# Kernel optimization log

Hardware: AMD Instinct MI355X
Metric: run time of the kernel (lower is better)

## Reference

```python
import jax, jax.numpy as jnp
import numpy as np

DEPTH = 10                      # levels per complete binary tree (node_order in [0, DEPTH-1])
N_TREES = 512
NODES_PER_TREE = 2 ** DEPTH - 1  # 1023
N_FEAT = 64
N_HIDDEN = 64


def _build_forest():
    """Forest of N_TREES complete binary trees, heap-indexed within each tree.

    node_order: 0 at leaves, DEPTH-1 at root (pytorch-tree-lstm convention).
    adjacency_list: (parent, child) pairs, parents grouped consecutively.
    edge_order: node_order of the parent of each edge.
    """
    npt = NODES_PER_TREE
    idx = np.arange(npt)
    level = np.floor(np.log2(idx + 1)).astype(np.int64)   # 0 at root
    order = (DEPTH - 1) - level                            # 0 at leaves
    internal = idx[2 * idx + 2 < npt]
    parents = np.repeat(internal, 2)
    children = np.empty_like(parents)
    children[0::2] = 2 * internal + 1
    children[1::2] = 2 * internal + 2
    base_adj = np.stack([parents, children], axis=1)       # [e, 2]
    eorder = order[parents]
    off = (np.arange(N_TREES) * npt).astype(np.int64)
    node_order = np.tile(order, N_TREES)
    adj = (base_adj[None, :, :] + off[:, None, None]).reshape(-1, 2)
    edge_order = np.tile(eorder, N_TREES)
    return node_order, adj, edge_order


def setup_inputs() -> dict:
    key = jax.random.key(0)
    ks = jax.random.split(key, 10)
    node_order, adj, edge_order = _build_forest()
    N = N_TREES * NODES_PER_TREE
    H, F = N_HIDDEN, N_FEAT
    s_in = 1.0 / np.sqrt(F)
    s_h = 1.0 / np.sqrt(H)
    return {
        "features": jax.random.normal(ks[0], (N, F), jnp.float32),
        "node_order": jnp.asarray(node_order),
        "adjacency_list": jnp.asarray(adj),
        "edge_order": jnp.asarray(edge_order),
        "w_iou": jax.random.normal(ks[1], (3 * H, F), jnp.float32) * s_in,
        "b_iou": jnp.zeros((3 * H,), jnp.float32),
        "u_iou": jax.random.normal(ks[2], (3 * H, H), jnp.float32) * s_h,
        "w_f": jax.random.normal(ks[3], (H, F), jnp.float32) * s_in,
        "b_f": jnp.zeros((H,), jnp.float32),
        "u_f": jax.random.normal(ks[4], (H, H), jnp.float32) * s_h,
        "lin0_w": jax.random.normal(ks[5], (H, H), jnp.float32) * s_h,
        "lin0_b": jnp.zeros((H,), jnp.float32),
        "lin1_w": jax.random.normal(ks[6], (H, H), jnp.float32) * s_h,
        "lin1_b": jnp.zeros((H,), jnp.float32),
        "out_w": jax.random.normal(ks[7], (1, H), jnp.float32) * s_h,
        "out_b": jnp.zeros((1,), jnp.float32),
    }


def _tree_lstm(features, node_order, parent, child, edge_order,
               w_iou, b_iou, u_iou, w_f, b_f, u_f):
    N = features.shape[0]
    H = u_f.shape[0]
    # input contributions are level-independent: compute once for all nodes
    iou_x = features @ w_iou.T + b_iou   # [N, 3H]
    f_x = features @ w_f.T + b_f         # [N, H]
    h = jnp.zeros((N, H), features.dtype)
    c = jnp.zeros((N, H), features.dtype)
    for n in range(DEPTH):               # dependency-chained level sweep
        nmask = (node_order == n)[:, None]
        emask = (edge_order == n)[:, None].astype(features.dtype)
        child_h = h[child]               # [E, H] gather
        child_c = c[child]
        # sum of children h per parent, restricted to this level's edges
        h_sum = jax.ops.segment_sum(child_h * emask, parent, num_segments=N)
        iou = iou_x + h_sum @ u_iou.T
        i, o, u = jnp.split(iou, 3, axis=1)
        i = jax.nn.sigmoid(i)
        o = jax.nn.sigmoid(o)
        u = jnp.tanh(u)
        # per-edge forget gates; contributions masked to this level's edges
        f = jax.nn.sigmoid(f_x[parent] + child_h @ u_f.T)
        c_sum = jax.ops.segment_sum(f * child_c * emask, parent, num_segments=N)
        c = jnp.where(nmask, i * u + c_sum, c)
        h = jnp.where(nmask, o * jnp.tanh(c), h)
    return h, c


def reference(features, node_order, adjacency_list, edge_order,
              w_iou, b_iou, u_iou, w_f, b_f, u_f,
              lin0_w, lin0_b, lin1_w, lin1_b, out_w, out_b):
    parent = adjacency_list[:, 0]
    child = adjacency_list[:, 1]
    h, _ = _tree_lstm(features, node_order, parent, child, edge_order,
                      w_iou, b_iou, u_iou, w_f, b_f, u_f)
    # unbatch + mean pool per tree (all trees have equal size -> reshape)
    x = h.reshape(N_TREES, NODES_PER_TREE, -1).mean(axis=1)
    x = jax.nn.relu(x)                   # dropout is identity in eval mode
    x = jax.nn.relu(x @ lin0_w.T + lin0_b)
    x = jax.nn.relu(x @ lin1_w.T + lin1_b)
    return (x @ out_w.T + out_b).ravel()  # [N_TREES]
```

## Files before the change

### kernel.cpp

```cpp
#include <hip/hip_runtime.h>
#include <math.h>

#define NTREES 512
#define DEPTH  10
#define NPT    1023
#define NTOT   (NTREES * NPT)
#define H      64
#define PART_SLOTS 32256

typedef __attribute__((ext_vector_type(8))) short bf16x8;
typedef __attribute__((ext_vector_type(4))) float f32x4;

__device__ __forceinline__ float sigm(float x)  { return __builtin_amdgcn_rcpf(1.0f + __expf(-x)); }
__device__ __forceinline__ float ftanh(float x) { return fmaf(-2.0f, __builtin_amdgcn_rcpf(__expf(2.0f * x) + 1.0f), 1.0f); }

__device__ __forceinline__ unsigned short bf_hi(float f) {
    unsigned u = __float_as_uint(f);
    return (unsigned short)((u + 0x7fffu + ((u >> 16) & 1u)) >> 16);
}
__device__ __forceinline__ float bf_f(unsigned short h) {
    return __uint_as_float(((unsigned)h) << 16);
}
__device__ __forceinline__ void split8(const float v[8], bf16x8& hi, bf16x8& lo) {
    #pragma unroll
    for (int e = 0; e < 8; ++e) {
        unsigned short hh = bf_hi(v[e]);
        hi[e] = (short)hh;
        lo[e] = (short)bf_hi(v[e] - bf_f(hh));
    }
}

#define MFMA(a, b, c) __builtin_amdgcn_mfma_f32_16x16x32_bf16((a), (b), (c), 0, 0, 0)

__global__ void prep_b(const float* __restrict__ w_iou, const float* __restrict__ u_iou,
                       const float* __restrict__ w_f,  const float* __restrict__ u_f,
                       unsigned short* __restrict__ B)
{
    int idx  = blockIdx.x * 256 + threadIdx.x;
    int unit = idx >> 3;
    int e    = idx & 7;
    int l    = unit & 63;
    float v;
    int hl;
    if (unit < 6144) {
        int sp = (unit >= 3072) ? 1 : 0;
        int r  = unit - sp * 3072;
        int q  = r >> 6;
        hl     = q & 1;
        int ts = q >> 1;
        int s_ = ts & 1;
        int t  = ts >> 1;
        int s  = sp * 2 + s_;
        int col = t * 16 + (l & 15);
        int k   = 32 * s + 8 * (l >> 4) + e;
        v = (k < 64) ? w_iou[col * H + k] : u_iou[col * H + (k - 64)];
    } else {
        int r  = unit - 6144;
        int q  = r >> 6;
        hl     = q & 1;
        int xu = (q >> 1) & 1;
        int ts = q >> 2;
        int s  = ts & 1;
        int t  = ts >> 1;
        int col = t * 16 + (l & 15);
        int k   = 32 * s + 8 * (l >> 4) + e;
        v = xu ? u_f[col * H + k] : w_f[col * H + k];
    }
    unsigned short hv = bf_hi(v);
    B[idx] = hl ? bf_hi(v - bf_f(hv)) : hv;
}

__device__ __forceinline__ void store_partial(float psum[4], int l, int wid,
                                              float* __restrict__ partw)
{
    #pragma unroll
    for (int t = 0; t < 4; ++t) {
        float v = psum[t];
        v += __shfl_xor(v, 16);
        v += __shfl_xor(v, 32);
        if (l < 16) partw[(size_t)wid * H + 16 * t + l] = v;
    }
}

__global__ __launch_bounds__(256, 3)
void leaf_mfma(const float* __restrict__ feat, const unsigned short* __restrict__ Braw,
               const float* __restrict__ b_iou,
               float* __restrict__ h, float* __restrict__ c,
               float* __restrict__ partw, int do_part)
{
    __shared__ bf16x8 Bs[3072];
    int tid = threadIdx.x;
    int l   = tid & 63;
    int w   = tid >> 6;
    int base = blockIdx.x * 64 + w * 16;
    int g    = base + (l & 15);
    int nrow = (g >> 9) * NPT + 511 + (g & 511);
    int ko   = 8 * (l >> 4);

    const float* fb = feat + (size_t)nrow * H + ko;
    float4 fr0 = *(const float4*)(fb);
    float4 fr1 = *(const float4*)(fb + 4);
    float4 fr2 = *(const float4*)(fb + 32);
    float4 fr3 = *(const float4*)(fb + 36);

    const bf16x8* Bg = (const bf16x8*)Braw;
    for (int u = tid; u < 3072; u += 256) Bs[u] = Bg[u];
    __syncthreads();

    bf16x8 fh[2], fl[2];
    { float v[8] = {fr0.x,fr0.y,fr0.z,fr0.w,fr1.x,fr1.y,fr1.z,fr1.w}; split8(v, fh[0], fl[0]); }
    { float v[8] = {fr2.x,fr2.y,fr2.z,fr2.w,fr3.x,fr3.y,fr3.z,fr3.w}; split8(v, fh[1], fl[1]); }

    f32x4 acc[12];
    #pragma unroll
    for (int t = 0; t < 12; ++t) acc[t] = (f32x4){0.f,0.f,0.f,0.f};
    #pragma unroll
    for (int t = 0; t < 12; ++t) {
        #pragma unroll
        for (int s = 0; s < 2; ++s) {
            bf16x8 bh = Bs[((t * 2 + s) * 2 + 0) * 64 + l];
            bf16x8 bl = Bs[((t * 2 + s) * 2 + 1) * 64 + l];
            acc[t] = MFMA(fh[s], bh, acc[t]);
            acc[t] = MFMA(fh[s], bl, acc[t]);
            acc[t] = MFMA(fl[s], bh, acc[t]);
        }
    }
    int colb = l & 15;
    float psum[4] = {0.f, 0.f, 0.f, 0.f};
    #pragma unroll
    for (int r = 0; r < 4; ++r) {
        int gr = base + (l >> 4) * 4 + r;
        int nr = (gr >> 9) * NPT + 511 + (gr & 511);
        #pragma unroll
        for (int t = 0; t < 4; ++t) {
            int j = 16 * t + colb;
            float ai = acc[t][r]     + b_iou[j];
            float ao = acc[4 + t][r] + b_iou[64 + j];
            float au = acc[8 + t][r] + b_iou[128 + j];
            float cv = sigm(ai) * ftanh(au);
            float hval = sigm(ao) * ftanh(cv);
            c[(size_t)nr * H + j] = cv;
            h[(size_t)nr * H + j] = hval;
            psum[t] += hval;
        }
    }
    if (do_part) store_partial(psum, l, blockIdx.x * 4 + w, partw);
}

__global__ __launch_bounds__(256, 3)
void internal_mfma(const float* __restrict__ feat, const unsigned short* __restrict__ Braw,
                   const float* __restrict__ b_iou, const float* __restrict__ b_f,
                   float* __restrict__ h, float* __restrict__ c, int lvl,
                   float* __restrict__ partw, int woff)
{
    __shared__ bf16x8 Bs[3072];
    int tid = threadIdx.x;
    int l   = tid & 63;
    int w   = tid >> 6;
    int m   = 1 << lvl;
    int base  = blockIdx.x * 64 + w * 16;
    int g     = base + (l & 15);
    int tree  = g >> lvl, i = g & (m - 1);
    int local = (m - 1) + i;
    int nrow  = tree * NPT + local;
    int crow0 = tree * NPT + 2 * local + 1;
    int ko    = 8 * (l >> 4);
    int colb  = l & 15;

    const float* fb  = feat + (size_t)nrow * H + ko;
    float4 fr0 = *(const float4*)(fb);
    float4 fr1 = *(const float4*)(fb + 4);
    float4 fr2 = *(const float4*)(fb + 32);
    float4 fr3 = *(const float4*)(fb + 36);
    const float* h0b = h + (size_t)crow0 * H + ko;
    const float* h1b = h0b + H;
    float4 a00 = *(const float4*)(h0b);
    float4 a01 = *(const float4*)(h0b + 4);
    float4 a02 = *(const float4*)(h0b + 32);
    float4 a03 = *(const float4*)(h0b + 36);
    float4 a10 = *(const float4*)(h1b);
    float4 a11 = *(const float4*)(h1b + 4);
    float4 a12 = *(const float4*)(h1b + 32);
    float4 a13 = *(const float4*)(h1b + 36);

    const bf16x8* Bg = (const bf16x8*)Braw;
    for (int u = tid; u < 2048; u += 256) Bs[u] = Bg[6144 + u];
    __syncthreads();

    bf16x8 fh[2], fl[2], sh[2], sl[2], zh[2], zl[2];
    { float v[8] = {fr0.x,fr0.y,fr0.z,fr0.w,fr1.x,fr1.y,fr1.z,fr1.w}; split8(v, fh[0], fl[0]); }
    { float v[8] = {fr2.x,fr2.y,fr2.z,fr2.w,fr3.x,fr3.y,fr3.z,fr3.w}; split8(v, fh[1], fl[1]); }
    {
        float v0[8] = {a00.x,a00.y,a00.z,a00.w,a01.x,a01.y,a01.z,a01.w};
        float v1[8] = {a10.x,a10.y,a10.z,a10.w,a11.x,a11.y,a11.z,a11.w};
        float vs[8];
        #pragma unroll
        for (int e = 0; e < 8; ++e) vs[e] = v0[e] + v1[e];
        split8(v0, zh[0], zl[0]); split8(vs, sh[0], sl[0]);
    }
    {
        float v0[8] = {a02.x,a02.y,a02.z,a02.w,a03.x,a03.y,a03.z,a03.w};
        float v1[8] = {a12.x,a12.y,a12.z,a12.w,a13.x,a13.y,a13.z,a13.w};
        float vs[8];
        #pragma unroll
        for (int e = 0; e < 8; ++e) vs[e] = v0[e] + v1[e];
        split8(v0, zh[1], zl[1]); split8(vs, sh[1], sl[1]);
    }

    float f0[4][4], f1[4][4];
    #pragma unroll
    for (int t = 0; t < 4; ++t) {
        f32x4 ax  = (f32x4){0.f,0.f,0.f,0.f};
        f32x4 as_ = (f32x4){0.f,0.f,0.f,0.f};
        f32x4 az  = (f32x4){0.f,0.f,0.f,0.f};
        #pragma unroll
        for (int s = 0; s < 2; ++s) {
            int qb = (t * 2 + s) * 4;
            bf16x8 bxh = Bs[(qb + 0) * 64 + l];
            bf16x8 bxl = Bs[(qb + 1) * 64 + l];
            bf16x8 buh = Bs[(qb + 2) * 64 + l];
            bf16x8 bul = Bs[(qb + 3) * 64 + l];
            ax  = MFMA(fh[s], bxh, ax);  ax  = MFMA(fh[s], bxl, ax);  ax  = MFMA(fl[s], bxh, ax);
            as_ = MFMA(sh[s], buh, as_); as_ = MFMA(sh[s], bul, as_); as_ = MFMA(sl[s], buh, as_);
            az  = MFMA(zh[s], buh, az);  az  = MFMA(zh[s], bul, az);  az  = MFMA(zl[s], buh, az);
        }
        #pragma unroll
        for (int r = 0; r < 4; ++r) {
            float afx = ax[r] + b_f[16 * t + colb];
            f0[t][r] = sigm(afx + az[r]);
            f1[t][r] = sigm(afx + (as_[r] - az[r]));
        }
    }
    __syncthreads();

    for (int u = tid; u < 3072; u += 256) Bs[u] = Bg[u];
    __syncthreads();
    f32x4 acc[12];
    #pragma unroll
    for (int t = 0; t < 12; ++t) acc[t] = (f32x4){0.f,0.f,0.f,0.f};
    #pragma unroll
    for (int t = 0; t < 12; ++t) {
        #pragma unroll
        for (int s = 0; s < 2; ++s) {
            bf16x8 bh = Bs[((t * 2 + s) * 2 + 0) * 64 + l];
            bf16x8 bl = Bs[((t * 2 + s) * 2 + 1) * 64 + l];
            acc[t] = MFMA(fh[s], bh, acc[t]);
            acc[t] = MFMA(fh[s], bl, acc[t]);
            acc[t] = MFMA(fl[s], bh, acc[t]);
        }
    }
    __syncthreads();

    for (int u = tid; u < 3072; u += 256) Bs[u] = Bg[3072 + u];
    __syncthreads();
    #pragma unroll
    for (int t = 0; t < 12; ++t) {
        #pragma unroll
        for (int s = 0; s < 2; ++s) {
            bf16x8 bh = Bs[((t * 2 + s) * 2 + 0) * 64 + l];
            bf16x8 bl = Bs[((t * 2 + s) * 2 + 1) * 64 + l];
            acc[t] = MFMA(sh[s], bh, acc[t]);
            acc[t] = MFMA(sh[s], bl, acc[t]);
            acc[t] = MFMA(sl[s], bh, acc[t]);
        }
    }

    float psum[4] = {0.f, 0.f, 0.f, 0.f};
    #pragma unroll
    for (int r = 0; r < 4; ++r) {
        int gr = base + (l >> 4) * 4 + r;
        int treer = gr >> lvl, ir = gr & (m - 1);
        int lr = (m - 1) + ir;
        int nr = treer * NPT + lr;
        size_t ch0 = (size_t)(treer * NPT + 2 * lr + 1) * H;
        size_t ch1 = ch0 + H;
        #pragma unroll
        for (int t = 0; t < 4; ++t) {
            int j = 16 * t + colb;
            float ai = acc[t][r]     + b_iou[j];
            float ao = acc[4 + t][r] + b_iou[64 + j];
            float au = acc[8 + t][r] + b_iou[128 + j];
            float cv = sigm(ai) * ftanh(au) + f0[t][r] * c[ch0 + j] + f1[t][r] * c[ch1 + j];
            float hval = sigm(ao) * ftanh(cv);
            c[(size_t)nr * H + j] = cv;
            h[(size_t)nr * H + j] = hval;
            psum[t] += hval;
        }
    }
    if (woff >= 0) store_partial(psum, l, woff + blockIdx.x * 4 + w, partw);
}

__global__ __launch_bounds__(64)
void final_mlp(const float* __restrict__ h, const float* __restrict__ partw,
               const float* __restrict__ l0w, const float* __restrict__ l0b,
               const float* __restrict__ l1w, const float* __restrict__ l1b,
               const float* __restrict__ ow,  const float* __restrict__ ob,
               float* __restrict__ out)
{
    int tree = blockIdx.x;
    int f = threadIdx.x;
    float s = 0.0f;
    #pragma unroll 4
    for (int k = 0; k < 32; ++k) s += partw[(size_t)(tree * 32 + k) * H + f];
    #pragma unroll 4
    for (int k = 0; k < 16; ++k) s += partw[(size_t)(16384 + tree * 16 + k) * H + f];
    #pragma unroll
    for (int k = 0; k < 8; ++k)  s += partw[(size_t)(24576 + tree * 8 + k) * H + f];
    #pragma unroll
    for (int k = 0; k < 4; ++k)  s += partw[(size_t)(28672 + tree * 4 + k) * H + f];
    #pragma unroll
    for (int k = 0; k < 2; ++k)  s += partw[(size_t)(30720 + tree * 2 + k) * H + f];
    s += partw[(size_t)(31744 + tree) * H + f];
    const float* hb = h + (size_t)tree * NPT * H;
    #pragma unroll
    for (int i = 0; i < 15; ++i) s += hb[i * H + f];
    float x = fmaxf(s * (1.0f / 1023.0f), 0.0f);

    __shared__ float xb[H];
    __shared__ float yb[H];
    xb[f] = x;
    __syncthreads();
    float acc = l0b[f];
    #pragma unroll
    for (int k = 0; k < H; ++k) acc = fmaf(l0w[f * H + k], xb[k], acc);
    acc = fmaxf(acc, 0.0f);
    yb[f] = acc;
    __syncthreads();
    float acc2 = l1b[f];
    #pragma unroll
    for (int k = 0; k < H; ++k) acc2 = fmaf(l1w[f * H + k], yb[k], acc2);
    acc2 = fmaxf(acc2, 0.0f);
    float t = ow[f] * acc2;
    #pragma unroll
    for (int off = 32; off > 0; off >>= 1) t += __shfl_down(t, off);
    if (f == 0) out[tree] = t + ob[0];
}

__global__ __launch_bounds__(256)
void pool_kernel(const float* __restrict__ h, float* __restrict__ x)
{
    __shared__ float red[4][H];
    int tree = blockIdx.x;
    int f = threadIdx.x & 63;
    int seg = threadIdx.x >> 6;
    const float* basep = h + (size_t)tree * NPT * H;
    int i0 = seg * 256, i1 = i0 + 256; if (i1 > NPT) i1 = NPT;
    float s = 0.f;
    for (int i = i0; i < i1; ++i) s += basep[i * H + f];
    red[seg][f] = s;
    __syncthreads();
    if (seg == 0) {
        float tot = red[0][f] + red[1][f] + red[2][f] + red[3][f];
        x[tree * H + f] = fmaxf(tot * (1.0f / 1023.0f), 0.0f);
    }
}

__global__ __launch_bounds__(64)
void mlp_kernel(const float* __restrict__ x,
                const float* __restrict__ l0w, const float* __restrict__ l0b,
                const float* __restrict__ l1w, const float* __restrict__ l1b,
                const float* __restrict__ ow,  const float* __restrict__ ob,
                float* __restrict__ out)
{
    int tree = blockIdx.x;
    int j = threadIdx.x;
    __shared__ float xb[H];
    __shared__ float yb[H];
    xb[j] = x[tree * H + j];
    __syncthreads();
    float acc = l0b[j];
    #pragma unroll
    for (int k = 0; k < H; ++k) acc = fmaf(l0w[j * H + k], xb[k], acc);
    acc = fmaxf(acc, 0.0f);
    yb[j] = acc;
    __syncthreads();
    float acc2 = l1b[j];
    #pragma unroll
    for (int k = 0; k < H; ++k) acc2 = fmaf(l1w[j * H + k], yb[k], acc2);
    acc2 = fmaxf(acc2, 0.0f);
    float t = ow[j] * acc2;
    #pragma unroll
    for (int off = 32; off > 0; off >>= 1) t += __shfl_down(t, off);
    if (j == 0) out[tree] = t + ob[0];
}

extern "C" void kernel_launch(void* const* d_in, const int* in_sizes, int n_in,
                              void* d_out, int out_size, void* d_ws, size_t ws_size,
                              hipStream_t stream)
{
    const float* feat  = (const float*)d_in[0];
    const float* w_iou = (const float*)d_in[4];
    const float* b_iou = (const float*)d_in[5];
    const float* u_iou = (const float*)d_in[6];
    const float* w_f   = (const float*)d_in[7];
    const float* b_f   = (const float*)d_in[8];
    const float* u_f   = (const float*)d_in[9];
    const float* l0w   = (const float*)d_in[10];
    const float* l0b   = (const float*)d_in[11];
    const float* l1w   = (const float*)d_in[12];
    const float* l1b   = (const float*)d_in[13];
    const float* ow    = (const float*)d_in[14];
    const float* ob    = (const float*)d_in[15];
    float* out = (float*)d_out;

    float* h = (float*)d_ws;
    float* c = h + (size_t)NTOT * H;
    float* x = c + (size_t)NTOT * H;
    unsigned short* Bf = (unsigned short*)(x + NTREES * H);
    float* partw = (float*)(Bf + 65536);
    size_t needed = (size_t)((char*)(partw + (size_t)PART_SLOTS * H) - (char*)d_ws);
    int use_part = (ws_size >= needed) ? 1 : 0;

    prep_b<<<256, 256, 0, stream>>>(w_iou, u_iou, w_f, u_f, Bf);
    leaf_mfma<<<4096, 256, 0, stream>>>(feat, Bf, b_iou, h, c, partw, use_part);
    for (int lvl = DEPTH - 2; lvl >= 0; --lvl) {
        int woff = (use_part && lvl >= 4) ? (32768 - (64 << lvl)) : -1;
        internal_mfma<<<8 << lvl, 256, 0, stream>>>(
            feat, Bf, b_iou, b_f, h, c, lvl, partw, woff);
    }
    if (use_part) {
        final_mlp<<<NTREES, 64, 0, stream>>>(h, partw, l0w, l0b, l1w, l1b, ow, ob, out);
    } else {
        pool_kernel<<<NTREES, 256, 0, stream>>>(h, x);
        mlp_kernel<<<NTREES, 64, 0, stream>>>(x, l0w, l0b, l1w, l1b, ow, ob, out);
    }
}
```

Before: 318.4 us.

## Fuse the four smallest tree levels into one persistent kernel

Replaces the four separate internal_mfma launches for tree levels 3..0 with one small_levels kernel of 32 blocks. Each block owns a fixed set of 16 trees, stages the full bf16 weight matrix in 128 KB of LDS, and steps through the levels with __syncthreads between them. This cuts three kernel launches and their gaps, plus repeated weight loads, on levels that have very little parallel work. The cost is low occupancy: only 32 blocks run, and at each lower level more warps sit idle.

```diff
diff --git a/kernel.cpp b/kernel.cpp
--- a/kernel.cpp
+++ b/kernel.cpp
@@ -290,6 +290,144 @@
     if (woff >= 0) store_partial(psum, l, woff + blockIdx.x * 4 + w, partw);
 }
 
+__global__ __launch_bounds__(512)
+void small_levels(const float* __restrict__ feat, const unsigned short* __restrict__ Braw,
+                  const float* __restrict__ b_iou, const float* __restrict__ b_f,
+                  float* __restrict__ h, float* __restrict__ c)
+{
+    extern __shared__ bf16x8 Bs[];
+    const bf16x8* Bg = (const bf16x8*)Braw;
+    int tid = threadIdx.x;
+    for (int u = tid; u < 8192; u += 512) Bs[u] = Bg[u];
+    __syncthreads();
+
+    int l    = tid & 63;
+    int w    = tid >> 6;
+    int colb = l & 15;
+    int ko   = 8 * (l >> 4);
+
+    for (int lvl = 3; lvl >= 0; --lvl) {
+        if (w < (1 << lvl)) {
+            int m     = 1 << lvl;
+            int base  = blockIdx.x * (16 << lvl) + w * 16;
+            int g     = base + colb;
+            int tree  = g >> lvl, i = g & (m - 1);
+            int local = (m - 1) + i;
+            int nrow  = tree * NPT + local;
+            int crow0 = tree * NPT + 2 * local + 1;
+
+            const float* fb  = feat + (size_t)nrow * H + ko;
+            float4 fr0 = *(const float4*)(fb);
+            float4 fr1 = *(const float4*)(fb + 4);
+            float4 fr2 = *(const float4*)(fb + 32);
+            float4 fr3 = *(const float4*)(fb + 36);
+            const float* h0b = h + (size_t)crow0 * H + ko;
+            const float* h1b = h0b + H;
+            float4 a00 = *(const float4*)(h0b);
+            float4 a01 = *(const float4*)(h0b + 4);
+            float4 a02 = *(const float4*)(h0b + 32);
+            float4 a03 = *(const float4*)(h0b + 36);
+            float4 a10 = *(const float4*)(h1b);
+            float4 a11 = *(const float4*)(h1b + 4);
+            float4 a12 = *(const float4*)(h1b + 32);
+            float4 a13 = *(const float4*)(h1b + 36);
+
+            bf16x8 fh[2], fl[2], sh[2], sl[2], zh[2], zl[2];
+            { float v[8] = {fr0.x,fr0.y,fr0.z,fr0.w,fr1.x,fr1.y,fr1.z,fr1.w}; split8(v, fh[0], fl[0]); }
+            { float v[8] = {fr2.x,fr2.y,fr2.z,fr2.w,fr3.x,fr3.y,fr3.z,fr3.w}; split8(v, fh[1], fl[1]); }
+            {
+                float v0[8] = {a00.x,a00.y,a00.z,a00.w,a01.x,a01.y,a01.z,a01.w};
+                float v1[8] = {a10.x,a10.y,a10.z,a10.w,a11.x,a11.y,a11.z,a11.w};
+                float vs[8];
+                #pragma unroll
+                for (int e = 0; e < 8; ++e) vs[e] = v0[e] + v1[e];
+                split8(v0, zh[0], zl[0]); split8(vs, sh[0], sl[0]);
+            }
+            {
+                float v0[8] = {a02.x,a02.y,a02.z,a02.w,a03.x,a03.y,a03.z,a03.w};
+                float v1[8] = {a12.x,a12.y,a12.z,a12.w,a13.x,a13.y,a13.z,a13.w};
+                float vs[8];
+                #pragma unroll
+                for (int e = 0; e < 8; ++e) vs[e] = v0[e] + v1[e];
+                split8(v0, zh[1], zl[1]); split8(vs, sh[1], sl[1]);
+            }
+
+            float f0[4][4], f1[4][4];
+            #pragma unroll
+            for (int t = 0; t < 4; ++t) {
+                f32x4 ax  = (f32x4){0.f,0.f,0.f,0.f};
+                f32x4 as_ = (f32x4){0.f,0.f,0.f,0.f};
+                f32x4 az  = (f32x4){0.f,0.f,0.f,0.f};
+                #pragma unroll
+                for (int s = 0; s < 2; ++s) {
+                    int qb = (t * 2 + s) * 4;
+                    bf16x8 bxh = Bs[6144 + (qb + 0) * 64 + l];
+                    bf16x8 bxl = Bs[6144 + (qb + 1) * 64 + l];
+                    bf16x8 buh = Bs[6144 + (qb + 2) * 64 + l];
+                    bf16x8 bul = Bs[6144 + (qb + 3) * 64 + l];
+                    ax  = MFMA(fh[s], bxh, ax);  ax  = MFMA(fh[s], bxl, ax);  ax  = MFMA(fl[s], bxh, ax);
+                    as_ = MFMA(sh[s], buh, as_); as_ = MFMA(sh[s], bul, as_); as_ = MFMA(sl[s], buh, as_);
+                    az  = MFMA(zh[s], buh, az);  az  = MFMA(zh[s], bul, az);  az  = MFMA(zl[s], buh, az);
+                }
+                #pragma unroll
+                for (int r = 0; r < 4; ++r) {
+                    float afx = ax[r] + b_f[16 * t + colb];
+                    f0[t][r] = sigm(afx + az[r]);
+                    f1[t][r] = sigm(afx + (as_[r] - az[r]));
+                }
+            }
+
+            f32x4 acc[12];
+            #pragma unroll
+            for (int t = 0; t < 12; ++t) acc[t] = (f32x4){0.f,0.f,0.f,0.f};
+            #pragma unroll
+            for (int t = 0; t < 12; ++t) {
+                #pragma unroll
+                for (int s = 0; s < 2; ++s) {
+                    bf16x8 bh = Bs[((t * 2 + s) * 2 + 0) * 64 + l];
+                    bf16x8 bl = Bs[((t * 2 + s) * 2 + 1) * 64 + l];
+                    acc[t] = MFMA(fh[s], bh, acc[t]);
+                    acc[t] = MFMA(fh[s], bl, acc[t]);
+                    acc[t] = MFMA(fl[s], bh, acc[t]);
+                }
+            }
+            #pragma unroll
+            for (int t = 0; t < 12; ++t) {
+                #pragma unroll
+                for (int s = 0; s < 2; ++s) {
+                    bf16x8 bh = Bs[3072 + ((t * 2 + s) * 2 + 0) * 64 + l];
+                    bf16x8 bl = Bs[3072 + ((t * 2 + s) * 2 + 1) * 64 + l];
+                    acc[t] = MFMA(sh[s], bh, acc[t]);
+                    acc[t] = MFMA(sh[s], bl, acc[t]);
+                    acc[t] = MFMA(sl[s], bh, acc[t]);
+                }
+            }
+
+            #pragma unroll
+            for (int r = 0; r < 4; ++r) {
+                int gr = base + (l >> 4) * 4 + r;
+                int treer = gr >> lvl, ir = gr & (m - 1);
+                int lr = (m - 1) + ir;
+                int nr = treer * NPT + lr;
+                size_t ch0 = (size_t)(treer * NPT + 2 * lr + 1) * H;
+                size_t ch1 = ch0 + H;
+                #pragma unroll
+                for (int t = 0; t < 4; ++t) {
+                    int j = 16 * t + colb;
+                    float ai = acc[t][r]     + b_iou[j];
+                    float ao = acc[4 + t][r] + b_iou[64 + j];
+                    float au = acc[8 + t][r] + b_iou[128 + j];
+                    float cv = sigm(ai) * ftanh(au) + f0[t][r] * c[ch0 + j] + f1[t][r] * c[ch1 + j];
+                    float hval = sigm(ao) * ftanh(cv);
+                    c[(size_t)nr * H + j] = cv;
+                    h[(size_t)nr * H + j] = hval;
+                }
+            }
+        }
+        __syncthreads();
+    }
+}
+
 __global__ __launch_bounds__(64)
 void final_mlp(const float* __restrict__ h, const float* __restrict__ partw,
                const float* __restrict__ l0w, const float* __restrict__ l0b,
@@ -411,13 +549,17 @@
     size_t needed = (size_t)((char*)(partw + (size_t)PART_SLOTS * H) - (char*)d_ws);
     int use_part = (ws_size >= needed) ? 1 : 0;
 
+    hipFuncSetAttribute(reinterpret_cast<const void*>(small_levels),
+                        hipFuncAttributeMaxDynamicSharedMemorySize, 131072);
+
     prep_b<<<256, 256, 0, stream>>>(w_iou, u_iou, w_f, u_f, Bf);
     leaf_mfma<<<4096, 256, 0, stream>>>(feat, Bf, b_iou, h, c, partw, use_part);
-    for (int lvl = DEPTH - 2; lvl >= 0; --lvl) {
-        int woff = (use_part && lvl >= 4) ? (32768 - (64 << lvl)) : -1;
+    for (int lvl = DEPTH - 2; lvl >= 4; --lvl) {
+        int woff = (use_part) ? (32768 - (64 << lvl)) : -1;
         internal_mfma<<<8 << lvl, 256, 0, stream>>>(
             feat, Bf, b_iou, b_f, h, c, lvl, partw, woff);
     }
+    small_levels<<<32, 512, 131072, stream>>>(feat, Bf, b_iou, b_f, h, c);
     if (use_part) {
         final_mlp<<<NTREES, 64, 0, stream>>>(h, partw, l0w, l0b, l1w, l1b, ow, ob, out);
     } else {
```

Result: faster. 303.0 us (-4.8%).
